# Performance work log

Measured on AMD Instinct MI355X. Metric: run time of the kernel, lower is better.

Reference implementation:

```python
import jax, jax.numpy as jnp
import numpy as np

N_NODES = 20000
N_EDGES = 640000
HID = 256
IN_F, IN_SIZE = 6, 6
OUT_F, FH = 6, 3
EDGE_DIM = 8
T_DIM, S_DIM = 4, 6
N_LAYERS = 5


def setup_inputs() -> dict:
    key = jax.random.key(0)
    ks = jax.random.split(key, 32)
    g = lambda i, shape, scale=0.05: jax.random.normal(ks[i], shape, dtype=jnp.float32) * scale
    inp = {
        "x": jax.random.normal(ks[0], (N_NODES, IN_F, IN_SIZE), dtype=jnp.float32),
        "edge_index": jax.random.randint(ks[1], (2, N_EDGES), 0, N_NODES, dtype=jnp.int32),
        "edge_attr": jax.random.normal(ks[2], (N_EDGES, EDGE_DIM), dtype=jnp.float32),
        "t": jax.random.normal(ks[3], (N_NODES, T_DIM), dtype=jnp.float32),
        "s": jax.random.normal(ks[4], (N_NODES, S_DIM), dtype=jnp.float32),
        # embedder
        "W_emb": g(5, (IN_F * IN_SIZE, HID)), "b_emb": jnp.zeros((HID,), jnp.float32),
        # spatio-temporal encoder: t/s linear embeds + fusion over concat(x, te, se)
        "W_t": g(6, (T_DIM, HID)), "b_t": jnp.zeros((HID,), jnp.float32),
        "W_s": g(7, (S_DIM, HID)), "b_s": jnp.zeros((HID,), jnp.float32),
        "W_f": g(8, (3 * HID, HID)), "b_f": jnp.zeros((HID,), jnp.float32),
        # layernorm
        "ln_g": jnp.ones((HID,), jnp.float32), "ln_b": jnp.zeros((HID,), jnp.float32),
        # 5 TransformerConv layers (heads=1): query/key/value/edge/skip linears
        "Wq": g(9, (N_LAYERS, HID, HID)), "bq": jnp.zeros((N_LAYERS, HID), jnp.float32),
        "Wk": g(10, (N_LAYERS, HID, HID)), "bk": jnp.zeros((N_LAYERS, HID), jnp.float32),
        "Wv": g(11, (N_LAYERS, HID, HID)), "bv": jnp.zeros((N_LAYERS, HID), jnp.float32),
        "We": g(12, (N_LAYERS, EDGE_DIM, HID)), "be": jnp.zeros((N_LAYERS, HID), jnp.float32),
        "Wskip": g(13, (N_LAYERS, HID, HID)), "bskip": jnp.zeros((N_LAYERS, HID), jnp.float32),
        # decoder
        "W_dec": g(14, (HID, OUT_F * FH)), "b_dec": jnp.zeros((OUT_F * FH,), jnp.float32),
    }
    return inp


def _layernorm(x, g, b, eps=1e-5):
    mu = jnp.mean(x, axis=-1, keepdims=True)
    var = jnp.mean((x - mu) ** 2, axis=-1, keepdims=True)
    return (x - mu) * jax.lax.rsqrt(var + eps) * g + b


def _transformer_conv(x, src, dst, edge_attr, Wq, bq, Wk, bk, Wv, bv, We, be, Wskip, bskip):
    n = x.shape[0]
    d = x.shape[1]
    q = x @ Wq + bq                      # [n, d]
    k = x @ Wk + bk
    v = x @ Wv + bv
    e = edge_attr @ We + be              # [E, d]
    kj = k[src] + e                      # gather + edge fuse [E, d]
    vj = v[src] + e
    alpha = jnp.sum(q[dst] * kj, axis=-1) / jnp.sqrt(jnp.float32(d))  # [E]
    # segment softmax over incoming edges of each destination node
    m = jax.ops.segment_max(alpha, dst, num_segments=n)
    a = jnp.exp(alpha - m[dst])
    denom = jax.ops.segment_sum(a, dst, num_segments=n)
    w = a / (denom[dst] + 1e-16)
    out = jax.ops.segment_sum(vj * w[:, None], dst, num_segments=n)  # [n, d]
    return out + x @ Wskip + bskip       # root/skip connection


def reference(x, edge_index, edge_attr, t, s,
              W_emb, b_emb, W_t, b_t, W_s, b_s, W_f, b_f, ln_g, ln_b,
              Wq, bq, Wk, bk, Wv, bv, We, be, Wskip, bskip, W_dec, b_dec):
    n = x.shape[0]
    h = x.reshape(n, -1) @ W_emb + b_emb
    te = t @ W_t + b_t
    se = s @ W_s + b_s
    h = jnp.concatenate([h, te, se], axis=-1) @ W_f + b_f   # spatio-temporal fuse
    h = jax.nn.relu(_layernorm(h, ln_g, ln_b))
    src, dst = edge_index[0], edge_index[1]
    for i in range(N_LAYERS):
        h = jax.nn.relu(_transformer_conv(h, src, dst, edge_attr,
                                          Wq[i], bq[i], Wk[i], bk[i], Wv[i], bv[i],
                                          We[i], be[i], Wskip[i], bskip[i]))
    out = h @ W_dec + b_dec
    return out.reshape(n, OUT_F, FH)
```

## Files before the change

kernel.cpp:

```cpp
#include <hip/hip_runtime.h>
#include <hip/hip_fp8.h>
#include <math.h>

#define NN 20000
#define NPAD 20096
#define NE 640000
#define NOUT 1152
#define GSS 272
#define KVB 512
#define CAP 80
#define SCQ 0.09016994f
#define ISCL 8.8057e-5f
#define TIDX(r,k) ((((r)>>4)*4096) + (((k)>>3)*128) + (((r)&15)*8) + ((k)&7))

typedef _Float16 f16;
typedef f16 f16x8 __attribute__((ext_vector_type(8)));
typedef f16 f16x4 __attribute__((ext_vector_type(4)));
typedef f16 h2    __attribute__((ext_vector_type(2)));
typedef float f32x4 __attribute__((ext_vector_type(4)));
typedef float f32x2 __attribute__((ext_vector_type(2)));

static __device__ __forceinline__ float fdot2(h2 a, h2 b, float c) {
#if __has_builtin(__builtin_amdgcn_fdot2)
  return __builtin_amdgcn_fdot2(a, b, c, false);
#else
  return c + (float)a[0]*(float)b[0] + (float)a[1]*(float)b[1];
#endif
}

static __device__ __forceinline__ float fast_exp2(float x) {
#if __has_builtin(__builtin_amdgcn_exp2f)
  return __builtin_amdgcn_exp2f(x);
#else
  return exp2f(x);
#endif
}

static __device__ __forceinline__ int sdot4(unsigned a, unsigned b, int c) {
#if __has_builtin(__builtin_amdgcn_sdot4)
  return __builtin_amdgcn_sdot4((int)a, (int)b, c, false);
#else
  int r = c;
  #pragma unroll
  for (int i = 0; i < 4; i++) {
    int ai = ((int)((a >> (8*i)) & 255) ^ 128) - 128;
    int bi = ((int)((b >> (8*i)) & 255) ^ 128) - 128;
    r += ai*bi;
  }
  return r;
#endif
}

static __device__ __forceinline__ unsigned pack_i8x4(float a, float b, float c, float d) {
  int i0 = (int)rintf(a), i1 = (int)rintf(b), i2 = (int)rintf(c), i3 = (int)rintf(d);
  i0 = max(-127, min(127, i0)); i1 = max(-127, min(127, i1));
  i2 = max(-127, min(127, i2)); i3 = max(-127, min(127, i3));
  return (unsigned)(i0 & 255) | ((unsigned)(i1 & 255) << 8)
       | ((unsigned)(i2 & 255) << 16) | ((unsigned)(i3 & 255) << 24);
}

static __device__ __forceinline__ unsigned pack_fp8x4(float a, float b, float c, float d) {
#if __has_builtin(__builtin_amdgcn_cvt_pk_fp8_f32)
  int r = __builtin_amdgcn_cvt_pk_fp8_f32(a, b, 0, false);
  r = __builtin_amdgcn_cvt_pk_fp8_f32(c, d, r, true);
  return (unsigned)r;
#else
  __hip_fp8_e4m3 w(a), x2(b), y(c), z(d);
  return (unsigned)w.__x | ((unsigned)x2.__x<<8) | ((unsigned)y.__x<<16) | ((unsigned)z.__x<<24);
#endif
}

template<bool HI>
static __device__ __forceinline__ f32x2 unpack_fp8x2(unsigned v) {
#if __has_builtin(__builtin_amdgcn_cvt_pk_f32_fp8)
  return __builtin_amdgcn_cvt_pk_f32_fp8((int)v, HI);
#else
  unsigned s = HI ? (v >> 16) : (v & 0xffff);
  __hip_fp8_e4m3 a, b; a.__x = (unsigned char)(s & 0xff); b.__x = (unsigned char)(s >> 8);
  return (f32x2){ (float)a, (float)b };
#endif
}

__global__ __launch_bounds__(256) void k_prep_all(
    const float* __restrict__ W_emb, const float* __restrict__ W_t,
    const float* __restrict__ W_s,   const float* __restrict__ W_f,
    const float* __restrict__ b_emb, const float* __restrict__ b_t,
    const float* __restrict__ b_s,   const float* __restrict__ b_f,
    const float* __restrict__ Wq, const float* __restrict__ Wk,
    const float* __restrict__ Wv, const float* __restrict__ Wsk,
    const float* __restrict__ We, const float* __restrict__ be,
    const float* __restrict__ bq, const float* __restrict__ bk,
    const float* __restrict__ bv, const float* __restrict__ bsk,
    f16* __restrict__ Wch, float* __restrict__ bc,
    f16* __restrict__ WT, float* __restrict__ b_all,
    f16* __restrict__ hA, f16* __restrict__ hB)
{
  __shared__ float smem[64*65];
  int b = blockIdx.x;
  int tid = threadIdx.x;

  if (b < 47) {
    int r = b, c = tid;
    if (r < 36) {
      float a = 0.f;
      for (int m = 0; m < 256; m++) a += W_emb[r*256+m] * W_f[m*256+c];
      Wch[r*256+c] = (f16)a;
    } else if (r < 40) {
      int rr = r - 36; float a = 0.f;
      for (int m = 0; m < 256; m++) a += W_t[rr*256+m] * W_f[(256+m)*256+c];
      Wch[r*256+c] = (f16)a;
    } else if (r < 46) {
      int rr = r - 40; float a = 0.f;
      for (int m = 0; m < 256; m++) a += W_s[rr*256+m] * W_f[(512+m)*256+c];
      Wch[r*256+c] = (f16)a;
    } else {
      float a = b_f[c];
      for (int m = 0; m < 256; m++) a += b_emb[m]*W_f[m*256+c];
      for (int m = 0; m < 256; m++) a += b_t[m]*W_f[(256+m)*256+c];
      for (int m = 0; m < 256; m++) a += b_s[m]*W_f[(512+m)*256+c];
      bc[c] = a;
    }
  } else if (b < 367) {
    float (*lds)[65] = (float(*)[65])smem;
    int bb = b - 47;
    int nt = bb & 3, kt = (bb >> 2) & 3, mat = (bb >> 4) & 3, L = bb >> 6;
    const float* src = (mat == 0 ? Wq : mat == 1 ? Wk : mat == 2 ? Wv : Wsk) + (size_t)L*65536;
    int k0 = kt*64, n0 = nt*64;
    int c = tid & 63, r4 = tid >> 6;
    #pragma unroll
    for (int rr = 0; rr < 16; rr++) {
      int row = rr*4 + r4;
      lds[row][c] = src[(size_t)(k0 + row)*256 + n0 + c];
    }
    __syncthreads();
    f16* dst = WT + (size_t)L*294912;
    int nl = tid & 63, kb2 = tid >> 6;
    int ng = mat*256 + n0 + nl;
    #pragma unroll
    for (int half = 0; half < 2; half++) {
      int kb = kb2 + half*4;
      f16x8 v;
      #pragma unroll
      for (int e = 0; e < 8; e++) v[e] = (f16)lds[kb*8 + e][nl];
      *(f16x8*)(dst + TIDX(ng, k0 + kb*8)) = v;
    }
  } else if (b < 412) {
    float* vec = smem;
    int bb = b - 367;
    int L = bb / 9;
    int t = bb % 9;
    vec[tid] = (t < 8) ? We[(size_t)L*2048 + t*256 + tid] : be[(size_t)L*256 + tid];
    __syncthreads();
    int wave = tid >> 6, lane = tid & 63;
    for (int k = wave; k < 256; k += 4) {
      f32x4 wq = *(const f32x4*)(Wq + (size_t)L*65536 + (size_t)k*256 + lane*4);
      f32x4 vv = *(const f32x4*)(vec + lane*4);
      float d = wq[0]*vv[0] + wq[1]*vv[1] + wq[2]*vv[2] + wq[3]*vv[3];
      #pragma unroll
      for (int o = 32; o; o >>= 1) d += __shfl_xor(d, o, 64);
      if (lane == 0) WT[(size_t)L*294912 + TIDX(1024 + t, k)] = (f16)d;
    }
  } else if (b < 417) {
    int L = b - 412;
    for (int c = tid; c < NOUT; c += 256) {
      float v;
      if (c < 256)       v = bq [L*256+c];
      else if (c < 512)  v = bk [L*256+(c-256)];
      else if (c < 768)  v = bv [L*256+(c-512)];
      else if (c < 1024) v = bsk[L*256+(c-768)];
      else if (c < 1032) {
        int t = c-1024; float a = 0.f;
        for (int m = 0; m < 256; m++) a += bq[L*256+m]*We[(size_t)L*2048 + t*256 + m];
        v = a;
      } else if (c == 1032) {
        float a = 0.f;
        for (int m = 0; m < 256; m++) a += bq[L*256+m]*be[L*256+m];
        v = a;
      } else v = 0.f;
      b_all[(size_t)L*NOUT + c] = v;
    }
  } else {
    f16* p = (b == 417 ? hA : hB) + (size_t)NN*256;
    f16x8 z = {};
    for (int i = tid; i < (NPAD-NN)*256/8; i += 256)
      *(f16x8*)(p + (size_t)i*8) = z;
  }
}

__global__ void k_scatter(const int* __restrict__ ei, const float* __restrict__ eattr,
                          int* cnt, int* __restrict__ src_s, f16* __restrict__ eaperm)
{
  int e = blockIdx.x*256 + threadIdx.x;
  if (e < NE) {
    int d = ei[NE + e];
    int pos = atomicAdd(&cnt[d], 1);
    int slot = d*CAP + pos;
    src_s[slot] = ei[e];
    f32x4 a0 = *(const f32x4*)(eattr + (size_t)e*8);
    f32x4 a1 = *(const f32x4*)(eattr + (size_t)e*8 + 4);
    f16x8 ea = { (f16)a0[0],(f16)a0[1],(f16)a0[2],(f16)a0[3],
                 (f16)a1[0],(f16)a1[1],(f16)a1[2],(f16)a1[3] };
    *(f16x8*)(eaperm + (size_t)slot*8) = ea;
  }
}

__global__ __launch_bounds__(256) void k_encoder(
    const float* __restrict__ x, const float* __restrict__ t, const float* __restrict__ s,
    const f16* __restrict__ Wch, const float* __restrict__ bc,
    const float* __restrict__ lng, const float* __restrict__ lnb,
    f16* __restrict__ h)
{
  __shared__ f16 Wcs[46*256];
  __shared__ float xin[16][48];
  __shared__ float bcs[256], lgs[256], lbs[256];
  int tid = threadIdx.x;
  int u0 = blockIdx.x * 16;
  for (int i = tid; i < 46*128; i += 256)
    ((unsigned int*)Wcs)[i] = ((const unsigned int*)Wch)[i];
  bcs[tid] = bc[tid]; lgs[tid] = lng[tid]; lbs[tid] = lnb[tid];
  for (int i = tid; i < 576; i += 256) xin[i/36][i%36] = x[(size_t)u0*36 + i];
  if (tid < 64) xin[tid>>2][36 + (tid&3)] = t[(size_t)u0*4 + tid];
  if (tid < 96) xin[tid/6][40 + tid%6] = s[(size_t)u0*6 + tid];
  __syncthreads();
  int node = tid >> 4, cg = tid & 15;
  int u = u0 + node;
  float acc[16];
  #pragma unroll
  for (int j = 0; j < 16; j++) acc[j] = bcs[cg*16+j];
  for (int r = 0; r < 46; r++) {
    float xv = xin[node][r];
    const h2* wr = (const h2*)(Wcs + r*256 + cg*16);
    #pragma unroll
    for (int j2 = 0; j2 < 8; j2++) {
      h2 w2 = wr[j2];
      acc[j2*2]   += xv * (float)w2[0];
      acc[j2*2+1] += xv * (float)w2[1];
    }
  }
  float sm = 0.f, sq = 0.f;
  #pragma unroll
  for (int j = 0; j < 16; j++) { sm += acc[j]; sq += acc[j]*acc[j]; }
  #pragma unroll
  for (int o = 1; o < 16; o <<= 1) { sm += __shfl_xor(sm, o, 64); sq += __shfl_xor(sq, o, 64); }
  float mu  = sm * (1.f/256.f);
  float var = sq * (1.f/256.f) - mu*mu;
  float rin = rsqrtf(var + 1e-5f);
  f16x8 o0, o1;
  #pragma unroll
  for (int j = 0; j < 8; j++) {
    int c = cg*16 + j;
    float v = (acc[j]-mu)*rin*lgs[c] + lbs[c];
    o0[j] = (f16)fmaxf(v, 0.f);
  }
  #pragma unroll
  for (int j = 0; j < 8; j++) {
    int c = cg*16 + 8 + j;
    float v = (acc[8+j]-mu)*rin*lgs[c] + lbs[c];
    o1[j] = (f16)fmaxf(v, 0.f);
  }
  *(f16x8*)(h + TIDX(u, cg*16))   = o0;
  *(f16x8*)(h + TIDX(u, cg*16+8)) = o1;
}

__global__ __launch_bounds__(256) void k_gemm(
    const f16* __restrict__ A, const f16* __restrict__ BT,
    const float* __restrict__ bias,
    unsigned char* __restrict__ qt8, unsigned char* __restrict__ kvt,
    f16* __restrict__ gsk)
{
  int tid = threadIdx.x;
  int wave = tid >> 6, lane = tid & 63;
  int wm = wave >> 1, wn = wave & 1;
  int bm = blockIdx.x * 128 + wm*64;
  int bn = blockIdx.y * 128 + wn*64;
  int lr = lane & 15;
  int kg = lane >> 4;
  f32x4 acc[4][4];
  #pragma unroll
  for (int i = 0; i < 4; i++)
    #pragma unroll
    for (int j = 0; j < 4; j++) acc[i][j] = (f32x4){0.f,0.f,0.f,0.f};

  const f16* Ab = A  + (size_t)(bm >> 4)*4096 + kg*128 + lr*8;
  const f16* Bb = BT + (size_t)(bn >> 4)*4096 + kg*128 + lr*8;
  #pragma unroll
  for (int k0 = 0; k0 < 256; k0 += 32) {
    f16x8 af[4], bf[4];
    #pragma unroll
    for (int i = 0; i < 4; i++) af[i] = *(const f16x8*)(Ab + i*4096 + k0*16);
    #pragma unroll
    for (int j = 0; j < 4; j++) bf[j] = *(const f16x8*)(Bb + j*4096 + k0*16);
    #pragma unroll
    for (int i = 0; i < 4; i++)
      #pragma unroll
      for (int j = 0; j < 4; j++)
        acc[i][j] = __builtin_amdgcn_mfma_f32_16x16x32_f16(bf[j], af[i], acc[i][j], 0, 0, 0);
  }

  #pragma unroll
  for (int j = 0; j < 4; j++) {
    int cb0 = bn + j*16;
    if (cb0 >= 1040) continue;
    int colq = cb0 + kg*4;
    f32x4 bv = *(const f32x4*)(bias + colq);
    #pragma unroll
    for (int i = 0; i < 4; i++) {
      int row = bm + i*16 + lr;
      float v0 = acc[i][j][0]+bv[0], v1 = acc[i][j][1]+bv[1];
      float v2 = acc[i][j][2]+bv[2], v3 = acc[i][j][3]+bv[3];
      if (cb0 < 256) {
        *(unsigned*)(qt8 + (size_t)row*256 + colq) = pack_i8x4(v0*32.f, v1*32.f, v2*32.f, v3*32.f);
      } else if (cb0 < 512) {
        *(unsigned*)(kvt + (size_t)row*KVB + (colq-256)) = pack_i8x4(v0*32.f, v1*32.f, v2*32.f, v3*32.f);
      } else if (cb0 < 768) {
        *(unsigned*)(kvt + (size_t)row*KVB + 256 + (colq-512)) = pack_fp8x4(v0, v1, v2, v3);
      } else if (cb0 < 1024) {
        f16x4 st = { (f16)v0, (f16)v1, (f16)v2, (f16)v3 };
        *(f16x4*)(gsk + (size_t)row*GSS + (colq-768)) = st;
      } else {
        f16x4 st = { (f16)(v0*SCQ), (f16)(v1*SCQ), (f16)(v2*SCQ), (f16)(v3*SCQ) };
        *(f16x4*)(gsk + (size_t)row*GSS + 256 + (colq-1024)) = st;
      }
    }
  }
}

__global__ __launch_bounds__(256) void k_attn(
    const unsigned char* __restrict__ qt8, const unsigned char* __restrict__ kvt,
    const f16* __restrict__ gsk, const f16* __restrict__ eaperm,
    const float* __restrict__ WeL, const float* __restrict__ beL,
    const int* __restrict__ cnt, const int* __restrict__ src_s,
    f16* __restrict__ hout, int n)
{
  __shared__ float mav[2][268];
  int wid  = threadIdx.x >> 6;
  int lane = threadIdx.x & 63;
  int nl   = wid >> 1;
  int wsub = wid & 1;
  int grp  = lane >> 4;
  int gl   = lane & 15;
  int u = blockIdx.x*2 + nl;
  bool active = (u < n);

  uint4 qp = {0,0,0,0};
  f16x8 qe8 = {};
  float qbv = 0.f;
  int deg = 0;
  if (active) {
    qp = *(const uint4*)(qt8 + (size_t)u*256 + gl*16);
    const f16* gb = gsk + (size_t)u*GSS;
    qe8 = *(const f16x8*)(gb + 256);
    qbv = (float)gb[264];
    deg = cnt[u];
  }

  float ssum = 0.f;
  float av[16];
  h2 ae2[4];
  #pragma unroll
  for (int j = 0; j < 16; j++) av[j] = 0.f;
  #pragma unroll
  for (int j = 0; j < 4; j++) ae2[j] = (h2){(f16)0.f, (f16)0.f};

  size_t ubase = (size_t)u*CAP;
  #pragma unroll 2
  for (int i = grp + wsub*4; i < deg; i += 8) {
    int sn = src_s[ubase + i];
    const unsigned char* kb = kvt + (size_t)sn*KVB;
    uint4 kw = *(const uint4*)(kb + gl*16);
    uint4 vw = *(const uint4*)(kb + 256 + gl*16);
    f16x8 ea = *(const f16x8*)(eaperm + (ubase + i)*8);

    int di = sdot4(kw.x, qp.x, 0);
    di = sdot4(kw.y, qp.y, di);
    di = sdot4(kw.z, qp.z, di);
    di = sdot4(kw.w, qp.w, di);
    di += __shfl_xor(di, 1, 64);
    di += __shfl_xor(di, 2, 64);
    di += __shfl_xor(di, 4, 64);
    di += __shfl_xor(di, 8, 64);

    float edot = 0.f;
    edot = fdot2((h2){ea[0],ea[1]}, (h2){qe8[0],qe8[1]}, edot);
    edot = fdot2((h2){ea[2],ea[3]}, (h2){qe8[2],qe8[3]}, edot);
    edot = fdot2((h2){ea[4],ea[5]}, (h2){qe8[4],qe8[5]}, edot);
    edot = fdot2((h2){ea[6],ea[7]}, (h2){qe8[6],qe8[7]}, edot);

    float w = fast_exp2((float)di*ISCL + edot + qbv);
    ssum += w;
    f32x2 p;
    p = unpack_fp8x2<false>(vw.x); av[0]  += w*p[0]; av[1]  += w*p[1];
    p = unpack_fp8x2<true >(vw.x); av[2]  += w*p[0]; av[3]  += w*p[1];
    p = unpack_fp8x2<false>(vw.y); av[4]  += w*p[0]; av[5]  += w*p[1];
    p = unpack_fp8x2<true >(vw.y); av[6]  += w*p[0]; av[7]  += w*p[1];
    p = unpack_fp8x2<false>(vw.z); av[8]  += w*p[0]; av[9]  += w*p[1];
    p = unpack_fp8x2<true >(vw.z); av[10] += w*p[0]; av[11] += w*p[1];
    p = unpack_fp8x2<false>(vw.w); av[12] += w*p[0]; av[13] += w*p[1];
    p = unpack_fp8x2<true >(vw.w); av[14] += w*p[0]; av[15] += w*p[1];
    f16 wh = (f16)w;
    h2 wv = {wh, wh};
    #pragma unroll
    for (int j = 0; j < 4; j++) ae2[j] += wv * (h2){ea[2*j], ea[2*j+1]};
  }

  float ae[8];
  #pragma unroll
  for (int j = 0; j < 4; j++) { ae[2*j] = (float)ae2[j][0]; ae[2*j+1] = (float)ae2[j][1]; }

  #pragma unroll
  for (int j = 0; j < 16; j++) {
    av[j] += __shfl_xor(av[j], 16, 64);
    av[j] += __shfl_xor(av[j], 32, 64);
  }
  #pragma unroll
  for (int j = 0; j < 8; j++) {
    ae[j] += __shfl_xor(ae[j], 16, 64);
    ae[j] += __shfl_xor(ae[j], 32, 64);
  }
  ssum += __shfl_xor(ssum, 16, 64);
  ssum += __shfl_xor(ssum, 32, 64);

  int cb = gl*16 + grp*4;
  if (wsub == 1 && active) {
    #pragma unroll
    for (int t = 0; t < 4; t++) mav[nl][cb+t] = av[grp*4+t];
    if (lane < 8) mav[nl][256+lane] = ae[lane];
    if (lane == 0) mav[nl][264] = ssum;
  }
  __syncthreads();
  if (wsub == 0 && active) {
    float s2 = ssum + mav[nl][264];
    float inv = 1.f/(s2 + 1e-16f);
    float aem[8];
    #pragma unroll
    for (int e = 0; e < 8; e++) aem[e] = ae[e] + mav[nl][256+e];
    const f16* gb = gsk + (size_t)u*GSS;
    f16 res[4];
    #pragma unroll
    for (int t = 0; t < 4; t++) {
      int c = cb + t;
      float o = av[grp*4+t] + mav[nl][c];
      #pragma unroll
      for (int e = 0; e < 8; e++) o += aem[e]*WeL[e*256 + c];
      o += s2*beL[c];
      o = o*inv + (float)gb[c];
      res[t] = (f16)fmaxf(o, 0.f);
    }
    f16x4 outp = { res[0], res[1], res[2], res[3] };
    *(f16x4*)(hout + TIDX(u, cb)) = outp;
  }
}

__global__ __launch_bounds__(256) void k_decoder(
    const f16* __restrict__ h, const float* __restrict__ Wd,
    const float* __restrict__ bd, float* __restrict__ out)
{
  int n0 = blockIdx.x*32;
  __shared__ float hs[32*256];
  int tid = threadIdx.x;
  for (int j = tid; j < 32*32; j += 256) {
    int node = j >> 5, c8 = (j & 31)*8;
    f16x8 v = *(const f16x8*)(h + TIDX(n0 + node, c8));
    float* dst = &hs[node*256 + c8];
    #pragma unroll
    for (int e = 0; e < 8; e++) dst[e] = (float)v[e];
  }
  __syncthreads();
  for (int o = tid; o < 32*18; o += 256) {
    int ln = o/18, col = o - ln*18;
    int node = n0 + ln;
    float acc = bd[col];
    const float* hr = &hs[ln*256];
    #pragma unroll 4
    for (int k4 = 0; k4 < 64; k4++) {
      f32x4 hv = *(const f32x4*)(hr + k4*4);
      acc += hv[0]*Wd[(k4*4+0)*18+col] + hv[1]*Wd[(k4*4+1)*18+col]
           + hv[2]*Wd[(k4*4+2)*18+col] + hv[3]*Wd[(k4*4+3)*18+col];
    }
    out[(size_t)node*18 + col] = acc;
  }
}

extern "C" void kernel_launch(void* const* d_in, const int* in_sizes, int n_in,
                              void* d_out, int out_size, void* d_ws, size_t ws_size,
                              hipStream_t stream)
{
  const float* x     = (const float*)d_in[0];
  const int*   ei    = (const int*)  d_in[1];
  const float* eattr = (const float*)d_in[2];
  const float* t     = (const float*)d_in[3];
  const float* s     = (const float*)d_in[4];
  const float* W_emb = (const float*)d_in[5];
  const float* b_emb = (const float*)d_in[6];
  const float* W_t   = (const float*)d_in[7];
  const float* b_t   = (const float*)d_in[8];
  const float* W_s   = (const float*)d_in[9];
  const float* b_s   = (const float*)d_in[10];
  const float* W_f   = (const float*)d_in[11];
  const float* b_f   = (const float*)d_in[12];
  const float* ln_g  = (const float*)d_in[13];
  const float* ln_b  = (const float*)d_in[14];
  const float* Wq    = (const float*)d_in[15];
  const float* bq    = (const float*)d_in[16];
  const float* Wk    = (const float*)d_in[17];
  const float* bk    = (const float*)d_in[18];
  const float* Wv    = (const float*)d_in[19];
  const float* bv    = (const float*)d_in[20];
  const float* We    = (const float*)d_in[21];
  const float* be    = (const float*)d_in[22];
  const float* Wsk   = (const float*)d_in[23];
  const float* bsk   = (const float*)d_in[24];
  const float* W_dec = (const float*)d_in[25];
  const float* b_dec = (const float*)d_in[26];

  float* wsf = (float*)d_ws;
  size_t off = 0;
  float* bc    = wsf + off; off += 256;
  float* b_all = wsf + off; off += (size_t)5*NOUT;
  f16*   Wch   = (f16*)(wsf + off); off += (size_t)46*256/2;
  f16*   WT    = (f16*)(wsf + off); off += (size_t)5*294912/2;
  unsigned char* qt8 = (unsigned char*)(wsf + off); off += (size_t)NPAD*256/4;
  unsigned char* kvt = (unsigned char*)(wsf + off); off += (size_t)NPAD*KVB/4;
  f16*   gsk   = (f16*)(wsf + off); off += (size_t)NPAD*GSS/2;
  f16*   hA    = (f16*)(wsf + off); off += (size_t)NPAD*256/2;
  f16*   hB    = (f16*)(wsf + off); off += (size_t)NPAD*256/2;
  f16*   eaperm= (f16*)(wsf + off); off += (size_t)NN*CAP*8/2;
  int*   src_s = (int*)(wsf + off); off += (size_t)NN*CAP;
  int*   cnt   = (int*)(wsf + off); off += NN;

  (void)hipMemsetAsync(cnt, 0, NN*sizeof(int), stream);
  k_prep_all<<<419, 256, 0, stream>>>(W_emb, W_t, W_s, W_f, b_emb, b_t, b_s, b_f,
                                      Wq, Wk, Wv, Wsk, We, be, bq, bk, bv, bsk,
                                      Wch, bc, WT, b_all, hA, hB);
  k_scatter <<<(NE+255)/256, 256, 0, stream>>>(ei, eattr, cnt, src_s, eaperm);

  k_encoder <<<NN/16, 256, 0, stream>>>(x, t, s, Wch, bc, ln_g, ln_b, hA);

  f16* hin = hA;
  f16* hot = hB;
  dim3 ggrid(NPAD/128, NOUT/128);
  for (int L = 0; L < 5; L++) {
    k_gemm<<<ggrid, 256, 0, stream>>>(hin, WT + (size_t)L*294912,
                                      b_all + (size_t)L*NOUT, qt8, kvt, gsk);
    k_attn<<<NN/2, 256, 0, stream>>>(qt8, kvt, gsk, eaperm, We + (size_t)L*2048,
                                     be + (size_t)L*256, cnt, src_s, hot, NN);
    f16* tmp = hin; hin = hot; hot = tmp;
  }
  k_decoder<<<NN/32, 256, 0, stream>>>(hin, W_dec, b_dec, (float*)d_out);
}
```

Measured before the change: 626.0 us.

## Split attention into per-edge alpha kernel and aggregation kernel; XCD-aware GEMM tile mapping

The fused attention kernel is split in two. k_alpha gives each lane one edge and computes the full 256-wide int8 dot product against the destination's query held in registers, then writes the exp weight to a new buffer. k_attn2 then gathers V and does the weighted aggregation with one wave per node, which removes the shared-memory cross-wave reduction and the block barrier. The GEMM launch is flattened to 1D and remapped so that consecutive tiles land on the same XCD for L2 locality. The cost is an extra kernel launch per layer, an extra global write and read of the per-edge weights, and K rows loaded as full 256-byte lines per lane, which is uncoalesced.

```diff
diff --git a/kernel.cpp b/kernel.cpp
--- a/kernel.cpp
+++ b/kernel.cpp
@@ -268,11 +268,18 @@
     unsigned char* __restrict__ qt8, unsigned char* __restrict__ kvt,
     f16* __restrict__ gsk)
 {
+  const int NWG = (NPAD/128)*9;
+  const int Q = NWG >> 3, R = NWG & 7;
+  int bid = blockIdx.x;
+  int xcd = bid & 7, jj = bid >> 3;
+  int wg = (xcd < R ? xcd*(Q+1) : R*(Q+1) + (xcd-R)*Q) + jj;
+  int bmt = wg / 9, bnt = wg - bmt*9;
+
   int tid = threadIdx.x;
   int wave = tid >> 6, lane = tid & 63;
   int wm = wave >> 1, wn = wave & 1;
-  int bm = blockIdx.x * 128 + wm*64;
-  int bn = blockIdx.y * 128 + wn*64;
+  int bm = bmt*128 + wm*64;
+  int bn = bnt*128 + wn*64;
   int lr = lane & 15;
   int kg = lane >> 4;
   f32x4 acc[4][4];
@@ -325,68 +332,74 @@
   }
 }
 
-__global__ __launch_bounds__(256) void k_attn(
+__global__ __launch_bounds__(256) void k_alpha(
     const unsigned char* __restrict__ qt8, const unsigned char* __restrict__ kvt,
     const f16* __restrict__ gsk, const f16* __restrict__ eaperm,
-    const float* __restrict__ WeL, const float* __restrict__ beL,
     const int* __restrict__ cnt, const int* __restrict__ src_s,
-    f16* __restrict__ hout, int n)
-{
-  __shared__ float mav[2][268];
-  int wid  = threadIdx.x >> 6;
-  int lane = threadIdx.x & 63;
-  int nl   = wid >> 1;
-  int wsub = wid & 1;
-  int grp  = lane >> 4;
-  int gl   = lane & 15;
-  int u = blockIdx.x*2 + nl;
-  bool active = (u < n);
-
-  uint4 qp = {0,0,0,0};
-  f16x8 qe8 = {};
-  float qbv = 0.f;
-  int deg = 0;
-  if (active) {
-    qp = *(const uint4*)(qt8 + (size_t)u*256 + gl*16);
-    const f16* gb = gsk + (size_t)u*GSS;
-    qe8 = *(const f16x8*)(gb + 256);
-    qbv = (float)gb[264];
-    deg = cnt[u];
-  }
-
-  float ssum = 0.f;
-  float av[16];
-  h2 ae2[4];
-  #pragma unroll
-  for (int j = 0; j < 16; j++) av[j] = 0.f;
-  #pragma unroll
-  for (int j = 0; j < 4; j++) ae2[j] = (h2){(f16)0.f, (f16)0.f};
-
-  size_t ubase = (size_t)u*CAP;
-  #pragma unroll 2
-  for (int i = grp + wsub*4; i < deg; i += 8) {
-    int sn = src_s[ubase + i];
-    const unsigned char* kb = kvt + (size_t)sn*KVB;
-    uint4 kw = *(const uint4*)(kb + gl*16);
-    uint4 vw = *(const uint4*)(kb + 256 + gl*16);
-    f16x8 ea = *(const f16x8*)(eaperm + (ubase + i)*8);
-
-    int di = sdot4(kw.x, qp.x, 0);
-    di = sdot4(kw.y, qp.y, di);
-    di = sdot4(kw.z, qp.z, di);
-    di = sdot4(kw.w, qp.w, di);
-    di += __shfl_xor(di, 1, 64);
-    di += __shfl_xor(di, 2, 64);
-    di += __shfl_xor(di, 4, 64);
-    di += __shfl_xor(di, 8, 64);
-
+    float* __restrict__ wbuf)
+{
+  int wid = threadIdx.x >> 6, lane = threadIdx.x & 63;
+  int u = __builtin_amdgcn_readfirstlane(blockIdx.x*4 + wid);
+  int deg = cnt[u];
+  const uint4* qp = (const uint4*)(qt8 + (size_t)u*256);
+  uint4 q[16];
+  #pragma unroll
+  for (int c = 0; c < 16; c++) q[c] = qp[c];
+  const f16* gb = gsk + (size_t)u*GSS;
+  f16x8 qe8 = *(const f16x8*)(gb + 256);
+  float qbv = (float)gb[264];
+  size_t ub = (size_t)u*CAP;
+  for (int i = lane; i < deg; i += 64) {
+    int sn = src_s[ub + i];
+    const uint4* kp = (const uint4*)(kvt + (size_t)sn*KVB);
+    int di = 0;
+    #pragma unroll
+    for (int c = 0; c < 16; c++) {
+      uint4 kw = kp[c];
+      di = sdot4(kw.x, q[c].x, di);
+      di = sdot4(kw.y, q[c].y, di);
+      di = sdot4(kw.z, q[c].z, di);
+      di = sdot4(kw.w, q[c].w, di);
+    }
+    f16x8 ea = *(const f16x8*)(eaperm + (ub + i)*8);
     float edot = 0.f;
     edot = fdot2((h2){ea[0],ea[1]}, (h2){qe8[0],qe8[1]}, edot);
     edot = fdot2((h2){ea[2],ea[3]}, (h2){qe8[2],qe8[3]}, edot);
     edot = fdot2((h2){ea[4],ea[5]}, (h2){qe8[4],qe8[5]}, edot);
     edot = fdot2((h2){ea[6],ea[7]}, (h2){qe8[6],qe8[7]}, edot);
-
-    float w = fast_exp2((float)di*ISCL + edot + qbv);
+    wbuf[ub + i] = fast_exp2((float)di*ISCL + edot + qbv);
+  }
+}
+
+__global__ __launch_bounds__(256) void k_attn2(
+    const unsigned char* __restrict__ kvt, const f16* __restrict__ gsk,
+    const f16* __restrict__ eaperm,
+    const float* __restrict__ WeL, const float* __restrict__ beL,
+    const int* __restrict__ cnt, const int* __restrict__ src_s,
+    const float* __restrict__ wbuf, f16* __restrict__ hout)
+{
+  int wid  = threadIdx.x >> 6;
+  int lane = threadIdx.x & 63;
+  int grp  = lane >> 4;
+  int gl   = lane & 15;
+  int u = blockIdx.x*4 + wid;
+  int deg = cnt[u];
+
+  float ssum = 0.f;
+  float av[16];
+  float ae[8];
+  #pragma unroll
+  for (int j = 0; j < 16; j++) av[j] = 0.f;
+  #pragma unroll
+  for (int j = 0; j < 8; j++) ae[j] = 0.f;
+
+  size_t ub = (size_t)u*CAP;
+  #pragma unroll 2
+  for (int i = grp; i < deg; i += 4) {
+    int sn = src_s[ub + i];
+    uint4 vw = *(const uint4*)(kvt + (size_t)sn*KVB + 256 + gl*16);
+    f16x8 ea = *(const f16x8*)(eaperm + (ub + i)*8);
+    float w = wbuf[ub + i];
     ssum += w;
     f32x2 p;
     p = unpack_fp8x2<false>(vw.x); av[0]  += w*p[0]; av[1]  += w*p[1];
@@ -397,15 +410,9 @@
     p = unpack_fp8x2<true >(vw.z); av[10] += w*p[0]; av[11] += w*p[1];
     p = unpack_fp8x2<false>(vw.w); av[12] += w*p[0]; av[13] += w*p[1];
     p = unpack_fp8x2<true >(vw.w); av[14] += w*p[0]; av[15] += w*p[1];
-    f16 wh = (f16)w;
-    h2 wv = {wh, wh};
-    #pragma unroll
-    for (int j = 0; j < 4; j++) ae2[j] += wv * (h2){ea[2*j], ea[2*j+1]};
-  }
-
-  float ae[8];
-  #pragma unroll
-  for (int j = 0; j < 4; j++) { ae[2*j] = (float)ae2[j][0]; ae[2*j+1] = (float)ae2[j][1]; }
+    #pragma unroll
+    for (int j = 0; j < 8; j++) ae[j] += w*(float)ea[j];
+  }
 
   #pragma unroll
   for (int j = 0; j < 16; j++) {
@@ -420,35 +427,22 @@
   ssum += __shfl_xor(ssum, 16, 64);
   ssum += __shfl_xor(ssum, 32, 64);
 
+  float inv = 1.f/(ssum + 1e-16f);
+  const f16* gb = gsk + (size_t)u*GSS;
   int cb = gl*16 + grp*4;
-  if (wsub == 1 && active) {
-    #pragma unroll
-    for (int t = 0; t < 4; t++) mav[nl][cb+t] = av[grp*4+t];
-    if (lane < 8) mav[nl][256+lane] = ae[lane];
-    if (lane == 0) mav[nl][264] = ssum;
-  }
-  __syncthreads();
-  if (wsub == 0 && active) {
-    float s2 = ssum + mav[nl][264];
-    float inv = 1.f/(s2 + 1e-16f);
-    float aem[8];
-    #pragma unroll
-    for (int e = 0; e < 8; e++) aem[e] = ae[e] + mav[nl][256+e];
-    const f16* gb = gsk + (size_t)u*GSS;
-    f16 res[4];
-    #pragma unroll
-    for (int t = 0; t < 4; t++) {
-      int c = cb + t;
-      float o = av[grp*4+t] + mav[nl][c];
-      #pragma unroll
-      for (int e = 0; e < 8; e++) o += aem[e]*WeL[e*256 + c];
-      o += s2*beL[c];
-      o = o*inv + (float)gb[c];
-      res[t] = (f16)fmaxf(o, 0.f);
-    }
-    f16x4 outp = { res[0], res[1], res[2], res[3] };
-    *(f16x4*)(hout + TIDX(u, cb)) = outp;
-  }
+  f16 res[4];
+  #pragma unroll
+  for (int t = 0; t < 4; t++) {
+    int c = cb + t;
+    float o = av[grp*4+t];
+    #pragma unroll
+    for (int e = 0; e < 8; e++) o += ae[e]*WeL[e*256 + c];
+    o += ssum*beL[c];
+    o = o*inv + (float)gb[c];
+    res[t] = (f16)fmaxf(o, 0.f);
+  }
+  f16x4 outp = { res[0], res[1], res[2], res[3] };
+  *(f16x4*)(hout + TIDX(u, cb)) = outp;
 }
 
 __global__ __launch_bounds__(256) void k_decoder(
@@ -526,6 +520,7 @@
   f16*   hB    = (f16*)(wsf + off); off += (size_t)NPAD*256/2;
   f16*   eaperm= (f16*)(wsf + off); off += (size_t)NN*CAP*8/2;
   int*   src_s = (int*)(wsf + off); off += (size_t)NN*CAP;
+  float* wbuf  = wsf + off; off += (size_t)NN*CAP;
   int*   cnt   = (int*)(wsf + off); off += NN;
 
   (void)hipMemsetAsync(cnt, 0, NN*sizeof(int), stream);
@@ -538,12 +533,12 @@
 
   f16* hin = hA;
   f16* hot = hB;
-  dim3 ggrid(NPAD/128, NOUT/128);
   for (int L = 0; L < 5; L++) {
-    k_gemm<<<ggrid, 256, 0, stream>>>(hin, WT + (size_t)L*294912,
-                                      b_all + (size_t)L*NOUT, qt8, kvt, gsk);
-    k_attn<<<NN/2, 256, 0, stream>>>(qt8, kvt, gsk, eaperm, We + (size_t)L*2048,
-                                     be + (size_t)L*256, cnt, src_s, hot, NN);
+    k_gemm<<<(NPAD/128)*9, 256, 0, stream>>>(hin, WT + (size_t)L*294912,
+                                             b_all + (size_t)L*NOUT, qt8, kvt, gsk);
+    k_alpha<<<NN/4, 256, 0, stream>>>(qt8, kvt, gsk, eaperm, cnt, src_s, wbuf);
+    k_attn2<<<NN/4, 256, 0, stream>>>(kvt, gsk, eaperm, We + (size_t)L*2048,
+                                      be + (size_t)L*256, cnt, src_s, wbuf, hot);
     f16* tmp = hin; hin = hot; hot = tmp;
   }
   k_decoder<<<NN/32, 256, 0, stream>>>(hin, W_dec, b_dec, (float*)d_out);
```

Result: faster. 581.9 us (-7.0%).
